# Optimization experiments

Hardware: AMD Instinct MI355X
Metric: run time of the kernel (lower is better)

The kernel has to match this reference:

```python
import jax, jax.numpy as jnp
import numpy as np

# Production-scale dims
B, S, D = 8, 2048, 1024          # batch, seq_len, d_model
E, ES, V = 32, 128, 1024         # n_experts, expert_size, v_dim (= d_model)
K = 4                            # top-k experts per token (n_heads)


def setup_inputs() -> dict:
    key = jax.random.key(0)
    k1, k2, k3, k4 = jax.random.split(key, 4)
    return {
        "x": jax.random.normal(k1, (B, S, D), jnp.float32),
        "keys": jax.random.normal(k2, (E, D, ES), jnp.float32) * (D ** -0.5),
        "values": jax.random.normal(k3, (E, ES, V), jnp.float32) * (ES ** -0.5),
        "expert_sel": jax.random.normal(k4, (E, D), jnp.float32) * (D ** -0.5),
    }


def reference(x, keys, values, expert_sel):
    """SigmaMoELayer forward (eval mode, sigmoid selection, no bias/dropout).
    Returns (out [B,S,V], reg_loss scalar)."""
    n_experts = expert_sel.shape[0]
    # Router logits: [B, S, E]
    sel_raw = jnp.einsum('bsd,ed->bse', x, expert_sel)

    # Entropy regularization: log_softmax over experts, log-mean over all tokens
    l = jax.nn.log_softmax(sel_raw.reshape(-1, n_experts), axis=-1)   # [T, E]
    lm = jax.scipy.special.logsumexp(l, axis=0) - jnp.log(jnp.asarray(l.shape[0], l.dtype))
    reg_loss = jnp.sum(lm * jnp.exp(lm))  # == -entropy_l(lm).mean()

    # Sigmoid gating + top-k expert selection
    sel = jax.nn.sigmoid(sel_raw)
    sel_val, sel_idx = jax.lax.top_k(sel, K)                          # [B,S,K]

    # Scatter gate values onto the expert axis: gate[b,s,e] = sel_val if e selected else 0
    gate = jnp.einsum('bske,bsk->bse',
                      jax.nn.one_hot(sel_idx, n_experts, dtype=x.dtype), sel_val)

    # Expert up-projection + ReLU, gated (relu(mask*z) == mask*relu(z), experts distinct)
    h = jax.nn.relu(jnp.einsum('bsd,edf->bsef', x, keys)) * gate[..., None]  # [B,S,E,ES]
    # Expert down-projection + combine across experts
    out = jnp.einsum('bsef,efv->bsv', h, values)                      # [B,S,V]
    return out, reg_loss
```

## Files before the change

### kernel.cpp

```cpp
#include <hip/hip_runtime.h>

typedef unsigned int uint;
typedef unsigned short ushort;

#define TT 16384
#define DD 1024
#define EE 32
#define ESS 128
#define VV 1024
#define KK 4
#define TILE 64
#define NTILE_MAX 1056
#define RSPLIT 8

typedef __attribute__((ext_vector_type(8))) short bf16x8;
typedef __attribute__((ext_vector_type(16))) float f32x16;

#define WS_SELRAW   0
#define WS_GATES    524288
#define WS_PGATE    589824
#define WS_STATS    655360
#define WS_LMSUMS   655360
#define WS_COUNTS   655392
#define WS_OFFSETS  655424
#define WS_CURSORS  655457
#define WS_NTILES   655489
#define WS_TMAPE    655490
#define WS_TMAPT    656546
#define WS_IDXS     657602
#define WS_PERM     723138
#define WS_XB       788736
#define WS_KF       9177344
#define WS_VF       11274496
#define WS_ISLOT    13371648
#define WS_STG      13437184
#define WS_NEED_U   46991616ull

__device__ __forceinline__ ushort f2b(float f) {
    uint u = __builtin_bit_cast(uint, f);
    u = (u + 0x7fffu + ((u >> 16) & 1u)) >> 16;
    return (ushort)u;
}
__device__ __forceinline__ uint bpack(float lo, float hi) {
    return (uint)f2b(lo) | ((uint)f2b(hi) << 16);
}
__device__ __forceinline__ float b2f(ushort b) {
    uint u = (uint)b << 16;
    return __builtin_bit_cast(float, u);
}

__device__ __forceinline__ void gload_lds16(const void* g, void* l) {
    __builtin_amdgcn_global_load_lds(
        (const __attribute__((address_space(1))) uint*)g,
        (__attribute__((address_space(3))) uint*)l, 16, 0, 0);
}

__global__ __launch_bounds__(256) void k_prep(const float* __restrict__ keys,
                                              const float* __restrict__ values,
                                              ushort* __restrict__ kfb,
                                              ushort* __restrict__ vfb) {
    const int l = threadIdx.x & 63;
    int b = blockIdx.x;
    if (b < EE * 64) {
        const int e = b >> 6, ks = b & 63;
        const int nf = threadIdx.x >> 6;
        const int f = nf * 32 + (l & 31);
        const int d0 = ks * 16 + (l >> 5) * 8;
        const float* src = keys + ((size_t)e * DD + d0) * ESS + f;
        float v[8];
#pragma unroll
        for (int j = 0; j < 8; j++) v[j] = src[(size_t)j * ESS];
        uint4 r = { bpack(v[0], v[1]), bpack(v[2], v[3]), bpack(v[4], v[5]), bpack(v[6], v[7]) };
        const size_t off = (((size_t)e * 64 + ks) * 4 + nf) * 512 + l * 8;
        *(uint4*)(kfb + off) = r;
    } else {
        b -= EE * 64;
        const int half = b & 1;
        const int env = b >> 1;
        const int e = env >> 5, nv = env & 31;
        const int ks = (threadIdx.x >> 6) + half * 4;
        const int v0 = nv * 32 + (l & 31);
        const int f0 = ks * 16 + (l >> 5) * 8;
        const float* src = values + ((size_t)e * ESS + f0) * VV + v0;
        float v[8];
#pragma unroll
        for (int j = 0; j < 8; j++) v[j] = src[(size_t)j * VV];
        uint4 r = { bpack(v[0], v[1]), bpack(v[2], v[3]), bpack(v[4], v[5]), bpack(v[6], v[7]) };
        const size_t off = (((size_t)e * 32 + nv) * 8 + ks) * 512 + l * 8;
        *(uint4*)(vfb + off) = r;
    }
}

__global__ __launch_bounds__(256) void k_router(const float* __restrict__ x,
                                                const float* __restrict__ sel,
                                                float* __restrict__ sel_part,
                                                uint* __restrict__ xbu,
                                                float* __restrict__ stats) {
    __shared__ float xs[64][68];
    __shared__ float ss[32][68];
    const int tid = threadIdx.x;
    if (blockIdx.x == 0 && blockIdx.y == 0 && tid < 64) stats[tid] = 0.f;
    const int t0 = blockIdx.x * 64;
    const int dch = blockIdx.y;
    const int el = tid & 31;
    const int tg = tid >> 5;
    float acc[8];
#pragma unroll
    for (int i = 0; i < 8; i++) acc[i] = 0.f;

    const int dlen = DD / RSPLIT;
    for (int dc = dch * dlen; dc < dch * dlen + dlen; dc += 64) {
#pragma unroll
        for (int i = 0; i < 4; i++) {
            int q = tid + 256 * i;
            int r = q >> 4, c4 = q & 15;
            size_t gi = (size_t)(t0 + r) * DD + dc + c4 * 4;
            float4 v = *(const float4*)&x[gi];
            *(float4*)&xs[r][c4 * 4] = v;
            uint2 bv = { bpack(v.x, v.y), bpack(v.z, v.w) };
            *(uint2*)&xbu[gi / 2] = bv;
        }
#pragma unroll
        for (int i = 0; i < 2; i++) {
            int q = tid + 256 * i;
            int e = q >> 4, c4 = q & 15;
            float4 v = *(const float4*)&sel[(size_t)e * DD + dc + c4 * 4];
            *(float4*)&ss[e][c4 * 4] = v;
        }
        __syncthreads();
#pragma unroll
        for (int d4 = 0; d4 < 16; d4++) {
            float4 sv = *(const float4*)&ss[el][d4 * 4];
#pragma unroll
            for (int i = 0; i < 8; i++) {
                float4 xv = *(const float4*)&xs[tg * 8 + i][d4 * 4];
                acc[i] += xv.x * sv.x + xv.y * sv.y + xv.z * sv.z + xv.w * sv.w;
            }
        }
        __syncthreads();
    }
    float* dst = sel_part + (size_t)dch * TT * EE;
#pragma unroll
    for (int i = 0; i < 8; i++)
        dst[(size_t)(t0 + tg * 8 + i) * EE + el] = acc[i];
}

__global__ __launch_bounds__(256) void k_token(const float* __restrict__ sel_part,
                                               float* __restrict__ gates,
                                               int* __restrict__ idxs,
                                               float* __restrict__ lm_sums,
                                               int* __restrict__ counts) {
    __shared__ int hist[EE];
    __shared__ float lmh[EE];
    const int tid = threadIdx.x;
    if (tid < EE) { hist[tid] = 0; lmh[tid] = 0.f; }
    __syncthreads();

    const int t = blockIdx.x * 256 + tid;
    float v[32];
#pragma unroll
    for (int j = 0; j < 8; j++) {
        float4 q[RSPLIT];
#pragma unroll
        for (int p = 0; p < RSPLIT; p++)
            q[p] = *(const float4*)&sel_part[((size_t)p * TT + t) * EE + j * 4];
        v[j * 4 + 0] = ((q[0].x + q[1].x) + (q[2].x + q[3].x)) + ((q[4].x + q[5].x) + (q[6].x + q[7].x));
        v[j * 4 + 1] = ((q[0].y + q[1].y) + (q[2].y + q[3].y)) + ((q[4].y + q[5].y) + (q[6].y + q[7].y));
        v[j * 4 + 2] = ((q[0].z + q[1].z) + (q[2].z + q[3].z)) + ((q[4].z + q[5].z) + (q[6].z + q[7].z));
        v[j * 4 + 3] = ((q[0].w + q[1].w) + (q[2].w + q[3].w)) + ((q[4].w + q[5].w) + (q[6].w + q[7].w));
    }
    float m = v[0];
#pragma unroll
    for (int e = 1; e < 32; e++) m = fmaxf(m, v[e]);
    float s = 0.f;
#pragma unroll
    for (int e = 0; e < 32; e++) s += expf(v[e] - m);
    const float lse = logf(s) + m;

    float sg[32];
#pragma unroll
    for (int e = 0; e < 32; e++) sg[e] = 1.f / (1.f + expf(-v[e]));

    unsigned taken = 0u;
#pragma unroll
    for (int k = 0; k < KK; k++) {
        float best = -1.f; int bi = 0;
#pragma unroll
        for (int e = 0; e < 32; e++) {
            bool free_e = !((taken >> e) & 1u);
            if (free_e && sg[e] > best) { best = sg[e]; bi = e; }
        }
        taken |= 1u << bi;
        gates[t * KK + k] = best;
        idxs[t * KK + k] = bi;
        atomicAdd(&hist[bi], 1);
    }

#pragma unroll
    for (int e = 0; e < 32; e++) {
        float pv = expf(v[e] - lse);
#pragma unroll
        for (int o = 32; o >= 1; o >>= 1) pv += __shfl_xor(pv, o, 64);
        if ((tid & 63) == 0) atomicAdd(&lmh[e], pv);
    }
    __syncthreads();
    if (tid < EE) {
        atomicAdd(&counts[tid], hist[tid]);
        atomicAdd(&lm_sums[tid], lmh[tid]);
    }
}

__global__ void k_scan(const int* __restrict__ counts, int* __restrict__ offsets,
                       int* __restrict__ cursors, int* __restrict__ tmape,
                       int* __restrict__ tmapt, int* __restrict__ ntiles,
                       const float* __restrict__ lm_sums, float* __restrict__ out_reg) {
    const int lane = threadIdx.x;
    int c = (lane < EE) ? counts[lane] : 0;
    int p = c;
#pragma unroll
    for (int o = 1; o < 32; o <<= 1) { int u = __shfl_up(p, o, 64); if (lane >= o) p += u; }
    const int off = p - c;
    if (lane < EE) { offsets[lane] = off; cursors[lane] = off; }
    if (lane == EE - 1) offsets[EE] = p;

    int nt = (c + TILE - 1) / TILE;
    int q = nt;
#pragma unroll
    for (int o = 1; o < 32; o <<= 1) { int u = __shfl_up(q, o, 64); if (lane >= o) q += u; }
    const int tb = q - nt;
    if (lane < EE)
        for (int j = 0; j < nt; j++) { tmape[tb + j] = lane; tmapt[tb + j] = j; }
    if (lane == EE - 1) ntiles[0] = q;

    float rv = 0.f;
    if (lane < EE) {
        float pe = lm_sums[lane] * (1.f / (float)TT);
        rv = pe * logf(pe);
    }
#pragma unroll
    for (int o = 16; o >= 1; o >>= 1) rv += __shfl_down(rv, o, 64);
    if (lane == 0) out_reg[0] = rv;
}

__global__ __launch_bounds__(256) void k_scatter(const int* __restrict__ idxs,
                                                 const float* __restrict__ gates,
                                                 int* __restrict__ cursors,
                                                 int* __restrict__ perm,
                                                 float* __restrict__ pgate,
                                                 int* __restrict__ islot) {
    __shared__ int lh[EE];
    __shared__ int lbase[EE];
    const int tid = threadIdx.x;
    if (tid < EE) lh[tid] = 0;
    __syncthreads();
    const int t = blockIdx.x * 256 + tid;
    int ee[KK], rk[KK];
#pragma unroll
    for (int k = 0; k < KK; k++) {
        ee[k] = idxs[t * KK + k];
        rk[k] = atomicAdd(&lh[ee[k]], 1);
    }
    __syncthreads();
    if (tid < EE) lbase[tid] = atomicAdd(&cursors[tid], lh[tid]);
    __syncthreads();
#pragma unroll
    for (int k = 0; k < KK; k++) {
        int pos = lbase[ee[k]] + rk[k];
        perm[pos] = t;
        pgate[pos] = gates[t * KK + k];
        islot[t * KK + k] = pos;
    }
}

template <bool STG>
__global__ __launch_bounds__(256, 3) void k_expert(
    const ushort* __restrict__ xb, const ushort* __restrict__ kfb,
    const ushort* __restrict__ vfb,
    const int* __restrict__ perm, const float* __restrict__ pgate,
    const int* __restrict__ offsets, const int* __restrict__ counts,
    const int* __restrict__ tmape, const int* __restrict__ tmapt,
    const int* __restrict__ ntiles, ushort* __restrict__ stg,
    float* __restrict__ out)
{
    __shared__ __align__(1024) char xsb[2][64 * 256];
    __shared__ __align__(16) ushort hs[64][128];
    __shared__ float gl[64];
    __shared__ int tl[64];

    const int bid = (blockIdx.x & 7) * 132 + (blockIdx.x >> 3);
    if (bid >= ntiles[0]) return;
    const int e = tmape[bid];
    const int base = offsets[e] + tmapt[bid] * TILE;
    const int nr = min(TILE, offsets[e] + counts[e] - base);
    const int tid = threadIdx.x;

    if (tid < 64) {
        int tok = 0; float g = 0.f;
        if (tid < nr) { tok = perm[base + tid]; g = pgate[base + tid]; }
        tl[tid] = tok; gl[tid] = g;
    }
    __syncthreads();

    const int lane = tid & 63, wid = tid >> 6;
    const int wm = wid >> 1, wn = wid & 1;
    const int l31 = lane & 31, l5 = lane >> 5;

    const char* xbytes = (const char*)xb;
    const ushort* kb = kfb + ((size_t)e * 256 + wn * 2) * 512 + lane * 8;

    int srow[4]; const char* ssrc[4];
#pragma unroll
    for (int i = 0; i < 4; i++) {
        srow[i] = wid * 4096 + i * 1024;
        int row = wid * 16 + i * 4 + (lane >> 4);
        int colb = (lane & 15) * 16;
        ssrc[i] = xbytes + (size_t)tl[row] * 2048 + (colb ^ ((row & 15) << 4));
    }

    f32x16 acc0, acc1;
#pragma unroll
    for (int r = 0; r < 16; r++) { acc0[r] = 0.f; acc1[r] = 0.f; }

#pragma unroll
    for (int i = 0; i < 4; i++)
        gload_lds16(ssrc[i], xsb[0] + srow[i]);

    bf16x8 b0p[8], b1p[8];
#pragma unroll
    for (int j = 0; j < 8; j++) {
        b0p[j] = *(const bf16x8*)(kb + (size_t)j * 2048);
        b1p[j] = *(const bf16x8*)(kb + (size_t)j * 2048 + 512);
    }
    asm volatile("s_waitcnt vmcnt(16)" ::: "memory");
    __builtin_amdgcn_s_barrier();
    __builtin_amdgcn_sched_barrier(0);

    const int hr = wm * 32 + l31;
    const int asw = (hr & 15) << 4;

    for (int c = 0; c < 8; c++) {
        const int cur = c & 1;
        if (c < 7) {
#pragma unroll
            for (int i = 0; i < 4; i++)
                gload_lds16(ssrc[i] + (c + 1) * 256, xsb[cur ^ 1] + srow[i]);
        }
        const char* xcur = xsb[cur];
#pragma unroll
        for (int ksl = 0; ksl < 8; ksl++) {
            bf16x8 a = *(const bf16x8*)(xcur + hr * 256 + ((ksl * 32 + l5 * 16) ^ asw));
            int ks = c * 8 + ksl;
            acc0 = __builtin_amdgcn_mfma_f32_32x32x16_bf16(a, b0p[ksl], acc0, 0, 0, 0);
            acc1 = __builtin_amdgcn_mfma_f32_32x32x16_bf16(a, b1p[ksl], acc1, 0, 0, 0);
            int nk = (ks + 8) & 63;
            b0p[ksl] = *(const bf16x8*)(kb + (size_t)nk * 2048);
            b1p[ksl] = *(const bf16x8*)(kb + (size_t)nk * 2048 + 512);
        }
        asm volatile("s_waitcnt vmcnt(16)" ::: "memory");
        __builtin_amdgcn_s_barrier();
        __builtin_amdgcn_sched_barrier(0);
    }

#pragma unroll
    for (int r = 0; r < 16; r++) {
        int row = (r & 3) + 8 * (r >> 2) + 4 * l5;
        int grow = wm * 32 + row;
        float g = gl[grow];
        int c0 = wn * 64 + l31;
        int c1 = c0 + 32;
        int sw = (grow & 7) << 3;
        hs[grow][c0 ^ sw] = f2b(fmaxf(acc0[r], 0.f) * g);
        hs[grow][c1 ^ sw] = f2b(fmaxf(acc1[r], 0.f) * g);
    }
    __syncthreads();

    bf16x8 af[8];
    const int hsw = (hr & 7) << 3;
#pragma unroll
    for (int ks = 0; ks < 8; ks++) {
        int cc = ks * 16 + l5 * 8;
        af[ks] = *(const bf16x8*)&hs[hr][cc ^ hsw];
    }

    const ushort* vb = vfb + ((size_t)e * 32 + wn * 16) * 4096 + lane * 8;
    bf16x8 vpa[4], vpb[4];
#pragma unroll
    for (int j = 0; j < 4; j++) {
        vpa[j] = *(const bf16x8*)(vb + (size_t)j * 512);
        vpb[j] = *(const bf16x8*)(vb + (size_t)(4 + j) * 512);
    }

#pragma unroll
    for (int nv = 0; nv < 16; nv++) {
        f32x16 acc;
#pragma unroll
        for (int r = 0; r < 16; r++) acc[r] = 0.f;
#pragma unroll
        for (int ks = 0; ks < 4; ks++)
            acc = __builtin_amdgcn_mfma_f32_32x32x16_bf16(af[ks], vpa[ks], acc, 0, 0, 0);
        if (nv < 15) {
#pragma unroll
            for (int j = 0; j < 4; j++)
                vpa[j] = *(const bf16x8*)(vb + ((size_t)(nv + 1) * 8 + j) * 512);
        }
#pragma unroll
        for (int ks = 0; ks < 4; ks++)
            acc = __builtin_amdgcn_mfma_f32_32x32x16_bf16(af[4 + ks], vpb[ks], acc, 0, 0, 0);
        if (nv < 15) {
#pragma unroll
            for (int j = 0; j < 4; j++)
                vpb[j] = *(const bf16x8*)(vb + ((size_t)(nv + 1) * 8 + 4 + j) * 512);
        }
        const int colb = wn * 512 + nv * 32 + l31;
#pragma unroll
        for (int r = 0; r < 16; r++) {
            int row = wm * 32 + (r & 3) + 8 * (r >> 2) + 4 * l5;
            if (row < nr) {
                if (STG)
                    stg[(size_t)(base + row) * VV + colb] = f2b(acc[r]);
                else
                    atomicAdd(&out[(size_t)tl[row] * VV + colb], acc[r]);
            }
        }
    }
}

__global__ __launch_bounds__(256) void k_combine(const ushort* __restrict__ stg,
                                                 const int* __restrict__ islot,
                                                 float* __restrict__ out) {
    const int tid = threadIdx.x;
    const int t = blockIdx.x * 2 + (tid >> 7);
    const int c8 = (tid & 127) * 8;
    const int4 sl = *(const int4*)&islot[t * KK];
    float acc[8];
#pragma unroll
    for (int j = 0; j < 8; j++) acc[j] = 0.f;
    const int slots[4] = { sl.x, sl.y, sl.z, sl.w };
#pragma unroll
    for (int k = 0; k < KK; k++) {
        bf16x8 v = *(const bf16x8*)(stg + (size_t)slots[k] * VV + c8);
#pragma unroll
        for (int j = 0; j < 8; j++) acc[j] += b2f((ushort)v[j]);
    }
    float4 o0 = { acc[0], acc[1], acc[2], acc[3] };
    float4 o1 = { acc[4], acc[5], acc[6], acc[7] };
    *(float4*)&out[(size_t)t * VV + c8] = o0;
    *(float4*)&out[(size_t)t * VV + c8 + 4] = o1;
}

extern "C" void kernel_launch(void* const* d_in, const int* in_sizes, int n_in,
                              void* d_out, int out_size, void* d_ws, size_t ws_size,
                              hipStream_t stream) {
    const float* x      = (const float*)d_in[0];
    const float* keys   = (const float*)d_in[1];
    const float* values = (const float*)d_in[2];
    const float* esel   = (const float*)d_in[3];
    float* out = (float*)d_out;

    float* wsf = (float*)d_ws;
    int*   wsi = (int*)d_ws;

    float* gates   = wsf + WS_GATES;
    float* pgate   = wsf + WS_PGATE;
    float* lm_sums = wsf + WS_LMSUMS;
    int*   counts  = wsi + WS_COUNTS;
    int*   offsets = wsi + WS_OFFSETS;
    int*   cursors = wsi + WS_CURSORS;
    int*   ntiles  = wsi + WS_NTILES;
    int*   tmape   = wsi + WS_TMAPE;
    int*   tmapt   = wsi + WS_TMAPT;
    int*   idxs    = wsi + WS_IDXS;
    int*   perm    = wsi + WS_PERM;
    int*   islot   = wsi + WS_ISLOT;
    uint*   xbu = (uint*)(wsf + WS_XB);
    ushort* xb  = (ushort*)xbu;
    ushort* kfb = (ushort*)(wsf + WS_KF);
    ushort* vfb = (ushort*)(wsf + WS_VF);
    ushort* stg = (ushort*)(wsf + WS_STG);

    const bool use_stg = ws_size >= WS_NEED_U * 4ull;
    float* sel_part = use_stg ? (float*)stg : (float*)kfb;

    if (!use_stg)
        hipMemsetAsync(d_out, 0, (size_t)TT * VV * sizeof(float), stream);

    k_router<<<dim3(TT / 64, RSPLIT), 256, 0, stream>>>(x, esel, sel_part, xbu,
                                                        wsf + WS_STATS);
    k_token<<<TT / 256, 256, 0, stream>>>(sel_part, gates, idxs, lm_sums, counts);

    k_prep<<<EE * 64 + EE * 64, 256, 0, stream>>>(keys, values, kfb, vfb);

    k_scan<<<1, 64, 0, stream>>>(counts, offsets, cursors, tmape, tmapt, ntiles,
                                 lm_sums, out + (size_t)TT * VV);
    k_scatter<<<TT / 256, 256, 0, stream>>>(idxs, gates, cursors, perm, pgate, islot);
    if (use_stg) {
        k_expert<true><<<NTILE_MAX, 256, 0, stream>>>(xb, kfb, vfb, perm, pgate,
                                                      offsets, counts, tmape, tmapt,
                                                      ntiles, stg, out);
        k_combine<<<TT / 2, 256, 0, stream>>>(stg, islot, out);
    } else {
        k_expert<false><<<NTILE_MAX, 256, 0, stream>>>(xb, kfb, vfb, perm, pgate,
                                                       offsets, counts, tmape, tmapt,
                                                       ntiles, stg, out);
    }
}
```

Measured before the change: 207.7 us.

## Split fused expert kernel into separate up-projection and down-projection kernels

```diff
diff --git a/kernel.cpp b/kernel.cpp
--- a/kernel.cpp
+++ b/kernel.cpp
@@ -35,6 +35,8 @@
 #define WS_ISLOT    13371648
 #define WS_STG      13437184
 #define WS_NEED_U   46991616ull
+#define WS_HAF      46991616
+#define WS_NEED2_U  51316992ull
 
 __device__ __forceinline__ ushort f2b(float f) {
     uint u = __builtin_bit_cast(uint, f);
@@ -269,6 +271,176 @@
         perm[pos] = t;
         pgate[pos] = gates[t * KK + k];
         islot[t * KK + k] = pos;
+    }
+}
+
+__global__ __launch_bounds__(256, 3) void k_exp1(
+    const ushort* __restrict__ xb, const ushort* __restrict__ kfb,
+    const int* __restrict__ perm, const float* __restrict__ pgate,
+    const int* __restrict__ offsets, const int* __restrict__ counts,
+    const int* __restrict__ tmape, const int* __restrict__ tmapt,
+    const int* __restrict__ ntiles, ushort* __restrict__ haf)
+{
+    __shared__ __align__(1024) char xsb[2][64 * 256];
+    __shared__ __align__(16) ushort hs[64][128];
+    __shared__ float gl[64];
+    __shared__ int tl[64];
+
+    const int bid = (blockIdx.x & 7) * 132 + (blockIdx.x >> 3);
+    if (bid >= ntiles[0]) return;
+    const int e = tmape[bid];
+    const int base = offsets[e] + tmapt[bid] * TILE;
+    const int nr = min(TILE, offsets[e] + counts[e] - base);
+    const int tid = threadIdx.x;
+
+    if (tid < 64) {
+        int tok = 0; float g = 0.f;
+        if (tid < nr) { tok = perm[base + tid]; g = pgate[base + tid]; }
+        tl[tid] = tok; gl[tid] = g;
+    }
+    __syncthreads();
+
+    const int lane = tid & 63, wid = tid >> 6;
+    const int wm = wid >> 1, wn = wid & 1;
+    const int l31 = lane & 31, l5 = lane >> 5;
+
+    const char* xbytes = (const char*)xb;
+    const ushort* kb = kfb + ((size_t)e * 256 + wn * 2) * 512 + lane * 8;
+
+    int srow[4]; const char* ssrc[4];
+#pragma unroll
+    for (int i = 0; i < 4; i++) {
+        srow[i] = wid * 4096 + i * 1024;
+        int row = wid * 16 + i * 4 + (lane >> 4);
+        int colb = (lane & 15) * 16;
+        ssrc[i] = xbytes + (size_t)tl[row] * 2048 + (colb ^ ((row & 15) << 4));
+    }
+
+    f32x16 acc0, acc1;
+#pragma unroll
+    for (int r = 0; r < 16; r++) { acc0[r] = 0.f; acc1[r] = 0.f; }
+
+#pragma unroll
+    for (int i = 0; i < 4; i++)
+        gload_lds16(ssrc[i], xsb[0] + srow[i]);
+
+    bf16x8 b0p[8], b1p[8];
+#pragma unroll
+    for (int j = 0; j < 8; j++) {
+        b0p[j] = *(const bf16x8*)(kb + (size_t)j * 2048);
+        b1p[j] = *(const bf16x8*)(kb + (size_t)j * 2048 + 512);
+    }
+    asm volatile("s_waitcnt vmcnt(16)" ::: "memory");
+    __builtin_amdgcn_s_barrier();
+    __builtin_amdgcn_sched_barrier(0);
+
+    const int hr = wm * 32 + l31;
+    const int asw = (hr & 15) << 4;
+
+    for (int c = 0; c < 8; c++) {
+        const int cur = c & 1;
+        if (c < 7) {
+#pragma unroll
+            for (int i = 0; i < 4; i++)
+                gload_lds16(ssrc[i] + (c + 1) * 256, xsb[cur ^ 1] + srow[i]);
+        }
+        const char* xcur = xsb[cur];
+#pragma unroll
+        for (int ksl = 0; ksl < 8; ksl++) {
+            bf16x8 a = *(const bf16x8*)(xcur + hr * 256 + ((ksl * 32 + l5 * 16) ^ asw));
+            int ks = c * 8 + ksl;
+            acc0 = __builtin_amdgcn_mfma_f32_32x32x16_bf16(a, b0p[ksl], acc0, 0, 0, 0);
+            acc1 = __builtin_amdgcn_mfma_f32_32x32x16_bf16(a, b1p[ksl], acc1, 0, 0, 0);
+            int nk = (ks + 8) & 63;
+            b0p[ksl] = *(const bf16x8*)(kb + (size_t)nk * 2048);
+            b1p[ksl] = *(const bf16x8*)(kb + (size_t)nk * 2048 + 512);
+        }
+        asm volatile("s_waitcnt vmcnt(16)" ::: "memory");
+        __builtin_amdgcn_s_barrier();
+        __builtin_amdgcn_sched_barrier(0);
+    }
+
+#pragma unroll
+    for (int r = 0; r < 16; r++) {
+        int row = (r & 3) + 8 * (r >> 2) + 4 * l5;
+        int grow = wm * 32 + row;
+        float g = gl[grow];
+        int c0 = wn * 64 + l31;
+        int c1 = c0 + 32;
+        int sw = (grow & 7) << 3;
+        hs[grow][c0 ^ sw] = f2b(fmaxf(acc0[r], 0.f) * g);
+        hs[grow][c1 ^ sw] = f2b(fmaxf(acc1[r], 0.f) * g);
+    }
+    __syncthreads();
+
+#pragma unroll
+    for (int q = 0; q < 4; q++) {
+        int cb = wid * 4 + q;
+        int rg = cb >> 3, ks = cb & 7;
+        int hrr = rg * 32 + l31;
+        int sw = (hrr & 7) << 3;
+        bf16x8 frag = *(const bf16x8*)&hs[hrr][(ks * 16 + l5 * 8) ^ sw];
+        *(bf16x8*)(haf + ((size_t)bid * 16 + cb) * 512 + lane * 8) = frag;
+    }
+}
+
+__global__ __launch_bounds__(256) void k_exp2(
+    const ushort* __restrict__ haf, const ushort* __restrict__ vfb,
+    const int* __restrict__ offsets, const int* __restrict__ counts,
+    const int* __restrict__ tmape, const int* __restrict__ tmapt,
+    const int* __restrict__ ntiles, ushort* __restrict__ stg)
+{
+    const int bid = (blockIdx.x & 7) * 132 + (blockIdx.x >> 3);
+    if (bid >= ntiles[0]) return;
+    const int e = tmape[bid];
+    const int base = offsets[e] + tmapt[bid] * TILE;
+    const int nr = min(TILE, offsets[e] + counts[e] - base);
+    const int tid = threadIdx.x;
+    const int lane = tid & 63, wid = tid >> 6;
+    const int wm = wid >> 1, wn = wid & 1;
+    const int l31 = lane & 31, l5 = lane >> 5;
+
+    bf16x8 af[8];
+#pragma unroll
+    for (int ks = 0; ks < 8; ks++)
+        af[ks] = *(const bf16x8*)(haf + ((size_t)bid * 16 + wm * 8 + ks) * 512 + lane * 8);
+
+    const ushort* vb = vfb + ((size_t)e * 32 + wn * 16) * 4096 + lane * 8;
+    bf16x8 vpa[4], vpb[4];
+#pragma unroll
+    for (int j = 0; j < 4; j++) {
+        vpa[j] = *(const bf16x8*)(vb + (size_t)j * 512);
+        vpb[j] = *(const bf16x8*)(vb + (size_t)(4 + j) * 512);
+    }
+
+#pragma unroll
+    for (int nv = 0; nv < 16; nv++) {
+        f32x16 acc;
+#pragma unroll
+        for (int r = 0; r < 16; r++) acc[r] = 0.f;
+#pragma unroll
+        for (int ks = 0; ks < 4; ks++)
+            acc = __builtin_amdgcn_mfma_f32_32x32x16_bf16(af[ks], vpa[ks], acc, 0, 0, 0);
+        if (nv < 15) {
+#pragma unroll
+            for (int j = 0; j < 4; j++)
+                vpa[j] = *(const bf16x8*)(vb + ((size_t)(nv + 1) * 8 + j) * 512);
+        }
+#pragma unroll
+        for (int ks = 0; ks < 4; ks++)
+            acc = __builtin_amdgcn_mfma_f32_32x32x16_bf16(af[4 + ks], vpb[ks], acc, 0, 0, 0);
+        if (nv < 15) {
+#pragma unroll
+            for (int j = 0; j < 4; j++)
+                vpb[j] = *(const bf16x8*)(vb + ((size_t)(nv + 1) * 8 + 4 + j) * 512);
+        }
+        const int colb = wn * 512 + nv * 32 + l31;
+#pragma unroll
+        for (int r = 0; r < 16; r++) {
+            int row = wm * 32 + (r & 3) + 8 * (r >> 2) + 4 * l5;
+            if (row < nr)
+                stg[(size_t)(base + row) * VV + colb] = f2b(acc[r]);
+        }
     }
 }
 
@@ -477,8 +649,10 @@
     ushort* kfb = (ushort*)(wsf + WS_KF);
     ushort* vfb = (ushort*)(wsf + WS_VF);
     ushort* stg = (ushort*)(wsf + WS_STG);
-
-    const bool use_stg = ws_size >= WS_NEED_U * 4ull;
+    ushort* haf = (ushort*)(wsf + WS_HAF);
+
+    const bool use_stg   = ws_size >= WS_NEED_U * 4ull;
+    const bool use_split = ws_size >= WS_NEED2_U * 4ull;
     float* sel_part = use_stg ? (float*)stg : (float*)kfb;
 
     if (!use_stg)
@@ -493,7 +667,14 @@
     k_scan<<<1, 64, 0, stream>>>(counts, offsets, cursors, tmape, tmapt, ntiles,
                                  lm_sums, out + (size_t)TT * VV);
     k_scatter<<<TT / 256, 256, 0, stream>>>(idxs, gates, cursors, perm, pgate, islot);
-    if (use_stg) {
+    if (use_split) {
+        k_exp1<<<NTILE_MAX, 256, 0, stream>>>(xb, kfb, perm, pgate,
+                                              offsets, counts, tmape, tmapt,
+                                              ntiles, haf);
+        k_exp2<<<NTILE_MAX, 256, 0, stream>>>(haf, vfb, offsets, counts,
+                                              tmape, tmapt, ntiles, stg);
+        k_combine<<<TT / 2, 256, 0, stream>>>(stg, islot, out);
+    } else if (use_stg) {
         k_expert<true><<<NTILE_MAX, 256, 0, stream>>>(xb, kfb, vfb, perm, pgate,
                                                       offsets, counts, tmape, tmapt,
                                                       ntiles, stg, out);
```

After: 217.6 us. 1.05x slower.
